# Performance work log

Measured on AMD Instinct MI355X. Metric: run time of the kernel, lower is better.

## Reference

```python
import jax, jax.numpy as jnp
import numpy as np

jax.config.update("jax_enable_x64", True)

B, S = 256, 256
TINY = float(np.finfo(np.float64).tiny)  # torch.finfo().tiny for double


def _matrix_tree_logZ(scores, mask):
    """scores: [B,S,S] float64, mask: [B,S] bool (col 0 is False).
    Returns sum over batch of log partition function (Matrix-Tree theorem)."""
    lens = mask.sum(-1)  # token counts per sentence (excludes root col)
    mask_r = mask.at[:, 0].set(True)  # index_fill(1, 0, 1)
    pair = mask_r[:, :, None] & mask_r[:, None, :]  # [B,S,S]
    s = jnp.where(pair, scores, -jnp.inf)
    m = jnp.max(s.reshape(s.shape[0], -1), axis=-1)  # [B] per-batch max for stability
    A = jnp.maximum(jnp.exp(s - m[:, None, None]), TINY)  # clamp like torch
    idx = jnp.arange(S)
    D = jnp.zeros_like(A).at[:, idx, idx].set(A.sum(-1))  # degree matrix
    eye = jnp.eye(S, dtype=A.dtype)
    # masked_scatter_: rows with mask_r True take (D - A) rows, else identity
    L = jnp.where(mask_r[:, :, None], D - A, eye)
    logZ = jnp.linalg.slogdet(L[:, 1:, 1:])[1] + m * lens
    return logZ.sum()


def setup_inputs() -> dict:
    key = jax.random.key(0)
    k1, k2 = jax.random.split(key)
    scores = jax.random.normal(k1, (B, S, S), dtype=jnp.float32)
    lens = jax.random.randint(k2, (B,), S // 2, S)  # sentence lengths
    pos = jnp.arange(S)
    # col 0 (pseudo root) False, padding beyond length False
    mask = (pos[None, :] >= 1) & (pos[None, :] < lens[:, None])
    return {"scores": scores, "mask": mask}


def reference(scores, mask):
    # mbr=True path: marginals = d logZ / d scores (computed in double like torch)
    s64 = scores.astype(jnp.float64)
    probs = jax.grad(_matrix_tree_logZ)(s64, mask)
    return probs.astype(jnp.float32)
```

## Files before the change

kernel.cpp:

```cpp
#include <hip/hip_runtime.h>
#include <math.h>


#define S 256
#define BB 256

__device__ __forceinline__ int rowmap(int lr, int kb) {
    int rt = lr >> 6;
    int rb = rt + (rt >= kb ? 1 : 0);
    return rb * 64 + (lr & 63);
}

__global__ __launch_bounds__(256) void k_max(const float* __restrict__ sc,
                                             float* __restrict__ partial) {
    int b = blockIdx.y, rg = blockIdx.x;
    const float4* p4 = (const float4*)(sc + (size_t)b * S * S + rg * 8192);
    int tid = threadIdx.x;
    float4 v[8];
    #pragma unroll
    for (int it = 0; it < 8; ++it) v[it] = p4[tid + 256 * it];
    float m = -1e30f;
    #pragma unroll
    for (int it = 0; it < 8; ++it)
        m = fmaxf(m, fmaxf(fmaxf(v[it].x, v[it].y), fmaxf(v[it].z, v[it].w)));
    for (int off = 32; off > 0; off >>= 1) m = fmaxf(m, __shfl_down(m, off));
    __shared__ float sm[4];
    if ((tid & 63) == 0) sm[tid >> 6] = m;
    __syncthreads();
    if (tid == 0) partial[b * 8 + rg] = fmaxf(fmaxf(sm[0], sm[1]), fmaxf(sm[2], sm[3]));
}

__global__ void k_n(const unsigned char* __restrict__ mk, const float* __restrict__ partial,
                    double* __restrict__ mb, int* __restrict__ nb) {
    int b = blockIdx.x, j = threadIdx.x;
    __shared__ int shc[4];

    const unsigned int* mw = (const unsigned int*)mk;
    unsigned int w0 = mw[0], w1 = mw[1];
    int mode = (w0 != 0u) ? 0 : ((w1 != 0u) ? 1 : 2);

    int c;
    if (mode == 0)      c = (mk[(size_t)b * S + j] != 0);
    else if (mode == 1) c = (((const int*)mk)[(size_t)b * S + j] != 0);
    else                c = (((const long long*)mk)[(size_t)b * S + j] != 0LL);

    int lane = j & 63, wid = j >> 6;
    int cs = c;
    for (int off = 32; off > 0; off >>= 1) cs += __shfl_down(cs, off);
    if (lane == 0) shc[wid] = cs;
    __syncthreads();
    if (j == 0) {
        nb[b] = shc[0] + shc[1] + shc[2] + shc[3];
        float mm = partial[b * 8];
        #pragma unroll
        for (int q = 1; q < 8; ++q) mm = fmaxf(mm, partial[b * 8 + q]);
        mb[b] = (double)mm;
    }
}

__global__ void k_build(const float* __restrict__ sc, const double* __restrict__ mb,
                        const int* __restrict__ nb, double* __restrict__ Mg) {
    int p = blockIdx.x, b = blockIdx.y, j = threadIdx.x;
    int n = nb[b];
    double* Mrow = Mg + ((size_t)b * S + p) * S;
    if (p >= n) {
        Mrow[j] = (j == p) ? 1.0 : 0.0;
        return;
    }
    __shared__ double se[S];
    __shared__ double shs[4];
    double m = mb[b];
    double e = (j <= n) ? (double)expf((float)((double)sc[((size_t)b * S + (p + 1)) * S + j] - m)) : 0.0;
    se[j] = e;
    int lane = j & 63, wid = j >> 6;
    double ssum = e;
    for (int off = 32; off > 0; off >>= 1) ssum += __shfl_down(ssum, off);
    if (lane == 0) shs[wid] = ssum;
    __syncthreads();
    double rowsum = shs[0] + shs[1] + shs[2] + shs[3];
    double v;
    if (j < n) v = ((j == p) ? rowsum : 0.0) - se[j + 1];
    else       v = (j == p) ? 1.0 : 0.0;
    Mrow[j] = v;
}

__global__ __launch_bounds__(256) void k_gjrow(double* __restrict__ Mg, double* __restrict__ Pg,
                                               int kb) {
    int b = blockIdx.x, tid = threadIdx.x;
    double* M = Mg + (size_t)b * S * S;
    double* P = Pg + (size_t)b * 4096;
    __shared__ double PT[64][66];
    __shared__ double Rs[64][200];
    __shared__ double rowbuf[64];
    __shared__ double colbuf[64];

    int i = tid >> 2, g = tid & 3, c0 = g << 4;
    double c[16];
    #pragma unroll
    for (int u = 0; u < 16; ++u)
        c[u] = M[(size_t)(kb * 64 + i) * S + kb * 64 + c0 + u];

    for (int kt = 0; kt < 4; ++kt) {
        #pragma unroll
        for (int ks = 0; ks < 16; ++ks) {
            int k = kt * 16 + ks;
            if (i == k) {
                #pragma unroll
                for (int u = 0; u < 16; ++u) rowbuf[c0 + u] = c[u];
            }
            if (g == kt) colbuf[i] = c[ks];
            __syncthreads();
            double pv = rowbuf[k];
            double f  = colbuf[i];
            double pivinv = 1.0 / pv;
            double rk[16];
            #pragma unroll
            for (int m2 = 0; m2 < 8; ++m2) {
                double2 t = *(const double2*)&rowbuf[c0 + 2 * m2];
                rk[2 * m2] = t.x; rk[2 * m2 + 1] = t.y;
            }
            if (i == k) {
                #pragma unroll
                for (int u = 0; u < 16; ++u)
                    c[u] = ((g == kt) && (u == ks)) ? pivinv : c[u] * pivinv;
            } else {
                double gm = f * pivinv;
                #pragma unroll
                for (int u = 0; u < 16; ++u)
                    c[u] = ((g == kt) && (u == ks)) ? (-gm) : fma(-gm, rk[u], c[u]);
            }
            __syncthreads();
        }
    }
    #pragma unroll
    for (int u = 0; u < 16; ++u) {
        PT[c0 + u][i] = c[u];
        P[i * 64 + c0 + u] = c[u];
        M[(size_t)(kb * 64 + i) * S + kb * 64 + c0 + u] = c[u];
    }
    {
        int cidx = tid & 63;
        #pragma unroll
        for (int rep = 0; rep < 16; ++rep) {
            int r = rep * 4 + (tid >> 6);
            #pragma unroll
            for (int cc = 0; cc < 3; ++cc) {
                int j = cc * 64 + cidx;
                Rs[r][j] = M[(size_t)(kb * 64 + r) * S + rowmap(j, kb)];
            }
        }
    }
    __syncthreads();

    int tx = tid & 15, ty = tid >> 4;
    double2 acc[4][6];
    #pragma unroll
    for (int q = 0; q < 4; ++q)
        #pragma unroll
        for (int w = 0; w < 6; ++w) acc[q][w] = double2{0.0, 0.0};

    for (int s = 0; s < 64; ++s) {
        double2 p01 = *(const double2*)&PT[s][4 * ty];
        double2 p23 = *(const double2*)&PT[s][4 * ty + 2];
        #pragma unroll
        for (int w = 0; w < 6; ++w) {
            double2 r = *(const double2*)&Rs[s][2 * tx + 32 * w];
            acc[0][w].x = fma(p01.x, r.x, acc[0][w].x); acc[0][w].y = fma(p01.x, r.y, acc[0][w].y);
            acc[1][w].x = fma(p01.y, r.x, acc[1][w].x); acc[1][w].y = fma(p01.y, r.y, acc[1][w].y);
            acc[2][w].x = fma(p23.x, r.x, acc[2][w].x); acc[2][w].y = fma(p23.x, r.y, acc[2][w].y);
            acc[3][w].x = fma(p23.y, r.x, acc[3][w].x); acc[3][w].y = fma(p23.y, r.y, acc[3][w].y);
        }
    }
    #pragma unroll
    for (int q = 0; q < 4; ++q) {
        size_t row = (size_t)(kb * 64 + 4 * ty + q) * S;
        #pragma unroll
        for (int w = 0; w < 6; ++w) {
            int j = 2 * tx + 32 * w;
            *(double2*)&M[row + rowmap(j, kb)] = acc[q][w];
        }
    }
}

__global__ __launch_bounds__(256) void k_int(double* __restrict__ Mg, int kb) {
    int id = blockIdx.x;
    int b = id >> 1, half = id & 1;
    double* M = Mg + (size_t)b * S * S;
    int tid = threadIdx.x;
    __shared__ double FTs[32][98];
    __shared__ double Rss[32][200];

    int tx = tid & 15, ty = tid >> 4;
    double2 acc[6][6];
    #pragma unroll
    for (int q = 0; q < 6; ++q)
        #pragma unroll
        for (int w = 0; w < 6; ++w) acc[q][w] = double2{0.0, 0.0};

    for (int ck = 0; ck < 2; ++ck) {
        __syncthreads();
        {
            int kk = tid & 31, lrb = (tid >> 5) * 12;
            #pragma unroll
            for (int q = 0; q < 12; ++q) {
                int lrg = half * 96 + lrb + q;
                FTs[kk][lrb + q] =
                    M[(size_t)rowmap(lrg, kb) * S + kb * 64 + ck * 32 + kk];
            }
            int jl = tid & 63, ss = tid >> 6;
            #pragma unroll
            for (int rep = 0; rep < 8; ++rep) {
                int kk2 = ss + 4 * rep;
                #pragma unroll
                for (int cc = 0; cc < 3; ++cc) {
                    int j = cc * 64 + jl;
                    Rss[kk2][j] = M[(size_t)(kb * 64 + ck * 32 + kk2) * S + rowmap(j, kb)];
                }
            }
        }
        __syncthreads();
        for (int kk = 0; kk < 32; ++kk) {
            double2 f01 = *(const double2*)&FTs[kk][6 * ty];
            double2 f23 = *(const double2*)&FTs[kk][6 * ty + 2];
            double2 f45 = *(const double2*)&FTs[kk][6 * ty + 4];
            #pragma unroll
            for (int w = 0; w < 6; ++w) {
                double2 r = *(const double2*)&Rss[kk][2 * tx + 32 * w];
                acc[0][w].x = fma(f01.x, r.x, acc[0][w].x); acc[0][w].y = fma(f01.x, r.y, acc[0][w].y);
                acc[1][w].x = fma(f01.y, r.x, acc[1][w].x); acc[1][w].y = fma(f01.y, r.y, acc[1][w].y);
                acc[2][w].x = fma(f23.x, r.x, acc[2][w].x); acc[2][w].y = fma(f23.x, r.y, acc[2][w].y);
                acc[3][w].x = fma(f23.y, r.x, acc[3][w].x); acc[3][w].y = fma(f23.y, r.y, acc[3][w].y);
                acc[4][w].x = fma(f45.x, r.x, acc[4][w].x); acc[4][w].y = fma(f45.x, r.y, acc[4][w].y);
                acc[5][w].x = fma(f45.y, r.x, acc[5][w].x); acc[5][w].y = fma(f45.y, r.y, acc[5][w].y);
            }
        }
    }
    #pragma unroll
    for (int q = 0; q < 6; ++q) {
        int lrg = half * 96 + ty * 6 + q;
        size_t row = (size_t)rowmap(lrg, kb) * S;
        #pragma unroll
        for (int w = 0; w < 6; ++w) {
            int j = 2 * tx + 32 * w;
            double* p = &M[row + rowmap(j, kb)];
            double2 old = *(double2*)p;
            *(double2*)p = double2{old.x - acc[q][w].x, old.y - acc[q][w].y};
        }
    }
}

__global__ __launch_bounds__(256) void k_colP(double* __restrict__ Mg,
                                              const double* __restrict__ Pg, int kb) {
    int b = blockIdx.x, tid = threadIdx.x;
    double* M = Mg + (size_t)b * S * S;
    const double* P = Pg + (size_t)b * 4096;
    __shared__ double FT2[64][194];
    __shared__ double Ps[64][66];
    {
        int k = tid & 63;
        #pragma unroll
        for (int rep = 0; rep < 48; ++rep) {
            int lr = rep * 4 + (tid >> 6);
            FT2[k][lr] = M[(size_t)rowmap(lr, kb) * S + kb * 64 + k];
        }
        #pragma unroll
        for (int rep = 0; rep < 16; ++rep) {
            int r = rep * 4 + (tid >> 6);
            Ps[r][k] = P[r * 64 + k];
        }
    }
    __syncthreads();
    int tx = tid & 15, ty = tid >> 4;
    double2 acc[12][2];
    #pragma unroll
    for (int q = 0; q < 12; ++q) { acc[q][0] = double2{0.0, 0.0}; acc[q][1] = double2{0.0, 0.0}; }

    for (int k = 0; k < 64; ++k) {
        double2 f[6];
        #pragma unroll
        for (int h = 0; h < 6; ++h) f[h] = *(const double2*)&FT2[k][12 * ty + 2 * h];
        double2 r0 = *(const double2*)&Ps[k][2 * tx];
        double2 r1 = *(const double2*)&Ps[k][2 * tx + 32];
        #pragma unroll
        for (int h = 0; h < 6; ++h) {
            acc[2 * h][0].x     = fma(f[h].x, r0.x, acc[2 * h][0].x);
            acc[2 * h][0].y     = fma(f[h].x, r0.y, acc[2 * h][0].y);
            acc[2 * h][1].x     = fma(f[h].x, r1.x, acc[2 * h][1].x);
            acc[2 * h][1].y     = fma(f[h].x, r1.y, acc[2 * h][1].y);
            acc[2 * h + 1][0].x = fma(f[h].y, r0.x, acc[2 * h + 1][0].x);
            acc[2 * h + 1][0].y = fma(f[h].y, r0.y, acc[2 * h + 1][0].y);
            acc[2 * h + 1][1].x = fma(f[h].y, r1.x, acc[2 * h + 1][1].x);
            acc[2 * h + 1][1].y = fma(f[h].y, r1.y, acc[2 * h + 1][1].y);
        }
    }
    #pragma unroll
    for (int q = 0; q < 12; ++q) {
        int lr = ty * 12 + q;
        size_t row = (size_t)rowmap(lr, kb) * S + kb * 64;
        #pragma unroll
        for (int w = 0; w < 2; ++w) {
            int u = 2 * tx + 32 * w;
            *(double2*)&M[row + u] = double2{-acc[q][w].x, -acc[q][w].y};
        }
    }
}

__global__ __launch_bounds__(256) void k_epi(const float* __restrict__ sc,
                                             const double* __restrict__ Mg,
                                             const double* __restrict__ mb,
                                             const int* __restrict__ nb,
                                             float* __restrict__ out) {
    int b = blockIdx.y;
    int t = blockIdx.x;
    int jj = t & 3, ii = t >> 2;
    int tid = threadIdx.x;
    int n = nb[b];
    double m = mb[b];
    const double* X = Mg + (size_t)b * S * S;
    __shared__ double Xs[64][33];
    __shared__ double sdiag[32];
    if (tid < 32) {
        int idx = 32 * ii + tid - 1;
        sdiag[tid] = (idx >= 0) ? X[(size_t)idx * S + idx] : 0.0;
    }
    {
        int c = tid >> 2, a0 = (tid & 3) << 3;
        int xr = 64 * jj + c - 1;
        #pragma unroll
        for (int u = 0; u < 8; ++u) {
            int a = a0 + u;
            int xc = 32 * ii + a - 1;
            Xs[c][a] = (xr >= 0 && xc >= 0) ? X[(size_t)xr * S + xc] : 0.0;
        }
    }
    __syncthreads();
    int cl = tid & 63, ag = tid >> 6;
    #pragma unroll
    for (int aa = 0; aa < 8; ++aa) {
        int a = ag * 8 + aa;
        int i = 32 * ii + a;
        int j = 64 * jj + cl;
        float v = 0.0f;
        if (i >= 1 && i <= n && j <= n) {
            double A = (double)expf((float)((double)sc[((size_t)b * S + i) * S + j] - m));
            double sub = (j >= 1) ? Xs[cl][a] : 0.0;
            v = (float)(A * (sdiag[a] - sub));
        }
        out[((size_t)b * S + i) * S + j] = v;
    }
}

extern "C" void kernel_launch(void* const* d_in, const int* in_sizes, int n_in,
                              void* d_out, int out_size, void* d_ws, size_t ws_size,
                              hipStream_t stream) {
    (void)in_sizes; (void)n_in; (void)out_size; (void)ws_size;
    const float* sc = (const float*)d_in[0];
    const unsigned char* mk = (const unsigned char*)d_in[1];
    double* ws = (double*)d_ws;

    double* M  = ws;
    double* P  = M + (size_t)BB * S * S;
    double* mb = P + (size_t)BB * 4096;
    int*    nb = (int*)(mb + BB);
    float*  partial = (float*)P;
    float*  out = (float*)d_out;

    k_max<<<dim3(8, BB), 256, 0, stream>>>(sc, partial);
    k_n<<<BB, 256, 0, stream>>>(mk, partial, mb, nb);
    k_build<<<dim3(S, BB), 256, 0, stream>>>(sc, mb, nb, M);
    for (int kb = 0; kb < 4; ++kb) {
        k_gjrow<<<BB, 256, 0, stream>>>(M, P, kb);
        k_int<<<2 * BB, 256, 0, stream>>>(M, kb);
        k_colP<<<BB, 256, 0, stream>>>(M, P, kb);
    }
    k_epi<<<dim3(32, BB), 256, 0, stream>>>(sc, M, mb, nb, out);
}
```

Measured before the change: 600.6 us.

## Rework build, GJ pivot sync, colP split, and epilogue transpose path

k_build now handles one row per wavefront (four rows per block) using wave shuffles instead of a cross-wave reduction. k_gjrow double-buffers the pivot row and column so each elimination step needs one barrier instead of two. k_colP is split across two blocks per batch with a K-chunked shared-memory tile, for more parallelism and less LDS per block. The epilogue becomes a transpose kernel that writes the inverse, cast to float, into the output buffer, followed by a vectorized float4 elementwise pass. That pass computes the subtracted term in float precision, which may cost some accuracy.

```diff
diff --git a/kernel.cpp b/kernel.cpp
--- a/kernel.cpp
+++ b/kernel.cpp
@@ -58,30 +58,39 @@
     }
 }
 
-__global__ void k_build(const float* __restrict__ sc, const double* __restrict__ mb,
-                        const int* __restrict__ nb, double* __restrict__ Mg) {
-    int p = blockIdx.x, b = blockIdx.y, j = threadIdx.x;
+__global__ __launch_bounds__(256) void k_build(const float* __restrict__ sc,
+                                               const double* __restrict__ mb,
+                                               const int* __restrict__ nb,
+                                               double* __restrict__ Mg) {
+    int b = blockIdx.y;
+    int wid = threadIdx.x >> 6, lane = threadIdx.x & 63;
+    int p = blockIdx.x * 4 + wid;
     int n = nb[b];
+    double m = mb[b];
+    __shared__ double se[4][260];
     double* Mrow = Mg + ((size_t)b * S + p) * S;
-    if (p >= n) {
-        Mrow[j] = (j == p) ? 1.0 : 0.0;
-        return;
-    }
-    __shared__ double se[S];
-    __shared__ double shs[4];
-    double m = mb[b];
-    double e = (j <= n) ? (double)expf((float)((double)sc[((size_t)b * S + (p + 1)) * S + j] - m)) : 0.0;
-    se[j] = e;
-    int lane = j & 63, wid = j >> 6;
-    double ssum = e;
+    bool act = (p < n);
+    double ssum = 0.0;
+    #pragma unroll
+    for (int c4 = 0; c4 < 4; ++c4) {
+        int j = lane + 64 * c4;
+        double ev = 0.0;
+        if (act && j <= n)
+            ev = (double)expf((float)((double)sc[((size_t)b * S + (p + 1)) * S + j] - m));
+        se[wid][j] = ev;
+        ssum += ev;
+    }
     for (int off = 32; off > 0; off >>= 1) ssum += __shfl_down(ssum, off);
-    if (lane == 0) shs[wid] = ssum;
+    ssum = __shfl(ssum, 0);
     __syncthreads();
-    double rowsum = shs[0] + shs[1] + shs[2] + shs[3];
-    double v;
-    if (j < n) v = ((j == p) ? rowsum : 0.0) - se[j + 1];
-    else       v = (j == p) ? 1.0 : 0.0;
-    Mrow[j] = v;
+    #pragma unroll
+    for (int c4 = 0; c4 < 4; ++c4) {
+        int j = lane + 64 * c4;
+        double v;
+        if (act && j < n) v = ((j == p) ? ssum : 0.0) - se[wid][j + 1];
+        else              v = (j == p) ? 1.0 : 0.0;
+        Mrow[j] = v;
+    }
 }
 
 __global__ __launch_bounds__(256) void k_gjrow(double* __restrict__ Mg, double* __restrict__ Pg,
@@ -91,8 +100,8 @@
     double* P = Pg + (size_t)b * 4096;
     __shared__ double PT[64][66];
     __shared__ double Rs[64][200];
-    __shared__ double rowbuf[64];
-    __shared__ double colbuf[64];
+    __shared__ double rbuf[2][64];
+    __shared__ double cbuf[2][64];
 
     int i = tid >> 2, g = tid & 3, c0 = g << 4;
     double c[16];
@@ -100,25 +109,27 @@
     for (int u = 0; u < 16; ++u)
         c[u] = M[(size_t)(kb * 64 + i) * S + kb * 64 + c0 + u];
 
+    if (i == 0) {
+        #pragma unroll
+        for (int u = 0; u < 16; ++u) rbuf[0][c0 + u] = c[u];
+    }
+    if (g == 0) cbuf[0][i] = c[0];
+
     for (int kt = 0; kt < 4; ++kt) {
         #pragma unroll
         for (int ks = 0; ks < 16; ++ks) {
             int k = kt * 16 + ks;
-            if (i == k) {
-                #pragma unroll
-                for (int u = 0; u < 16; ++u) rowbuf[c0 + u] = c[u];
-            }
-            if (g == kt) colbuf[i] = c[ks];
+            const int par = ks & 1;
             __syncthreads();
-            double pv = rowbuf[k];
-            double f  = colbuf[i];
+            double pv = rbuf[par][k];
+            double f  = cbuf[par][i];
+            double rk[16];
+            #pragma unroll
+            for (int m2 = 0; m2 < 8; ++m2) {
+                double2 t = *(const double2*)&rbuf[par][c0 + 2 * m2];
+                rk[2 * m2] = t.x; rk[2 * m2 + 1] = t.y;
+            }
             double pivinv = 1.0 / pv;
-            double rk[16];
-            #pragma unroll
-            for (int m2 = 0; m2 < 8; ++m2) {
-                double2 t = *(const double2*)&rowbuf[c0 + 2 * m2];
-                rk[2 * m2] = t.x; rk[2 * m2 + 1] = t.y;
-            }
             if (i == k) {
                 #pragma unroll
                 for (int u = 0; u < 16; ++u)
@@ -129,7 +140,12 @@
                 for (int u = 0; u < 16; ++u)
                     c[u] = ((g == kt) && (u == ks)) ? (-gm) : fma(-gm, rk[u], c[u]);
             }
-            __syncthreads();
+            if (i == k + 1) {
+                #pragma unroll
+                for (int u = 0; u < 16; ++u) rbuf[par ^ 1][c0 + u] = c[u];
+            }
+            if (ks < 15) { if (g == kt)     cbuf[par ^ 1][i] = c[ks + 1]; }
+            else         { if (g == kt + 1) cbuf[par ^ 1][i] = c[0]; }
         }
     }
     #pragma unroll
@@ -251,52 +267,57 @@
 
 __global__ __launch_bounds__(256) void k_colP(double* __restrict__ Mg,
                                               const double* __restrict__ Pg, int kb) {
-    int b = blockIdx.x, tid = threadIdx.x;
+    int id = blockIdx.x;
+    int b = id >> 1, half = id & 1;
     double* M = Mg + (size_t)b * S * S;
     const double* P = Pg + (size_t)b * 4096;
-    __shared__ double FT2[64][194];
-    __shared__ double Ps[64][66];
-    {
-        int k = tid & 63;
-        #pragma unroll
-        for (int rep = 0; rep < 48; ++rep) {
-            int lr = rep * 4 + (tid >> 6);
-            FT2[k][lr] = M[(size_t)rowmap(lr, kb) * S + kb * 64 + k];
-        }
-        #pragma unroll
-        for (int rep = 0; rep < 16; ++rep) {
-            int r = rep * 4 + (tid >> 6);
-            Ps[r][k] = P[r * 64 + k];
-        }
-    }
-    __syncthreads();
+    int tid = threadIdx.x;
+    __shared__ double FTs[32][98];
+    __shared__ double Ps[32][66];
+
     int tx = tid & 15, ty = tid >> 4;
-    double2 acc[12][2];
-    #pragma unroll
-    for (int q = 0; q < 12; ++q) { acc[q][0] = double2{0.0, 0.0}; acc[q][1] = double2{0.0, 0.0}; }
-
-    for (int k = 0; k < 64; ++k) {
-        double2 f[6];
-        #pragma unroll
-        for (int h = 0; h < 6; ++h) f[h] = *(const double2*)&FT2[k][12 * ty + 2 * h];
-        double2 r0 = *(const double2*)&Ps[k][2 * tx];
-        double2 r1 = *(const double2*)&Ps[k][2 * tx + 32];
-        #pragma unroll
-        for (int h = 0; h < 6; ++h) {
-            acc[2 * h][0].x     = fma(f[h].x, r0.x, acc[2 * h][0].x);
-            acc[2 * h][0].y     = fma(f[h].x, r0.y, acc[2 * h][0].y);
-            acc[2 * h][1].x     = fma(f[h].x, r1.x, acc[2 * h][1].x);
-            acc[2 * h][1].y     = fma(f[h].x, r1.y, acc[2 * h][1].y);
-            acc[2 * h + 1][0].x = fma(f[h].y, r0.x, acc[2 * h + 1][0].x);
-            acc[2 * h + 1][0].y = fma(f[h].y, r0.y, acc[2 * h + 1][0].y);
-            acc[2 * h + 1][1].x = fma(f[h].y, r1.x, acc[2 * h + 1][1].x);
-            acc[2 * h + 1][1].y = fma(f[h].y, r1.y, acc[2 * h + 1][1].y);
-        }
-    }
-    #pragma unroll
-    for (int q = 0; q < 12; ++q) {
-        int lr = ty * 12 + q;
-        size_t row = (size_t)rowmap(lr, kb) * S + kb * 64;
+    double2 acc[6][2];
+    #pragma unroll
+    for (int q = 0; q < 6; ++q) { acc[q][0] = double2{0.0, 0.0}; acc[q][1] = double2{0.0, 0.0}; }
+
+    for (int ck = 0; ck < 2; ++ck) {
+        __syncthreads();
+        {
+            int kk = tid & 31, lrb = (tid >> 5) * 12;
+            #pragma unroll
+            for (int q = 0; q < 12; ++q) {
+                int lrg = half * 96 + lrb + q;
+                FTs[kk][lrb + q] =
+                    M[(size_t)rowmap(lrg, kb) * S + kb * 64 + ck * 32 + kk];
+            }
+            int u = tid & 63;
+            #pragma unroll
+            for (int rep = 0; rep < 8; ++rep) {
+                int r = rep * 4 + (tid >> 6);
+                Ps[r][u] = P[(ck * 32 + r) * 64 + u];
+            }
+        }
+        __syncthreads();
+        for (int kk = 0; kk < 32; ++kk) {
+            double2 f01 = *(const double2*)&FTs[kk][6 * ty];
+            double2 f23 = *(const double2*)&FTs[kk][6 * ty + 2];
+            double2 f45 = *(const double2*)&FTs[kk][6 * ty + 4];
+            #pragma unroll
+            for (int w = 0; w < 2; ++w) {
+                double2 r = *(const double2*)&Ps[kk][2 * tx + 32 * w];
+                acc[0][w].x = fma(f01.x, r.x, acc[0][w].x); acc[0][w].y = fma(f01.x, r.y, acc[0][w].y);
+                acc[1][w].x = fma(f01.y, r.x, acc[1][w].x); acc[1][w].y = fma(f01.y, r.y, acc[1][w].y);
+                acc[2][w].x = fma(f23.x, r.x, acc[2][w].x); acc[2][w].y = fma(f23.x, r.y, acc[2][w].y);
+                acc[3][w].x = fma(f23.y, r.x, acc[3][w].x); acc[3][w].y = fma(f23.y, r.y, acc[3][w].y);
+                acc[4][w].x = fma(f45.x, r.x, acc[4][w].x); acc[4][w].y = fma(f45.x, r.y, acc[4][w].y);
+                acc[5][w].x = fma(f45.y, r.x, acc[5][w].x); acc[5][w].y = fma(f45.y, r.y, acc[5][w].y);
+            }
+        }
+    }
+    #pragma unroll
+    for (int q = 0; q < 6; ++q) {
+        int lrg = half * 96 + ty * 6 + q;
+        size_t row = (size_t)rowmap(lrg, kb) * S + kb * 64;
         #pragma unroll
         for (int w = 0; w < 2; ++w) {
             int u = 2 * tx + 32 * w;
@@ -305,49 +326,63 @@
     }
 }
 
-__global__ __launch_bounds__(256) void k_epi(const float* __restrict__ sc,
-                                             const double* __restrict__ Mg,
-                                             const double* __restrict__ mb,
-                                             const int* __restrict__ nb,
-                                             float* __restrict__ out) {
+__global__ __launch_bounds__(256) void k_xt(const double* __restrict__ Mg,
+                                            float* __restrict__ outF,
+                                            double* __restrict__ Dg) {
+    int b = blockIdx.y, t = blockIdx.x;
+    int r = t & 3, c = t >> 2;
+    const double* M = Mg + (size_t)b * S * S;
+    __shared__ float L[64][65];
+    int tid = threadIdx.x;
+    int cc = tid & 63;
+    #pragma unroll
+    for (int rep = 0; rep < 16; ++rep) {
+        int rr = rep * 4 + (tid >> 6);
+        L[rr][cc] = (float)M[(size_t)(64 * r + rr) * S + 64 * c + cc];
+    }
+    if (r == c && tid < 64)
+        Dg[(size_t)b * S + 64 * r + tid] = M[(size_t)(64 * r + tid) * S + 64 * r + tid];
+    __syncthreads();
+    int pp = tid & 63;
+    #pragma unroll
+    for (int rep = 0; rep < 16; ++rep) {
+        int qq = rep * 4 + (tid >> 6);
+        int orow = 64 * c + qq + 1, ocol = 64 * r + pp + 1;
+        if (orow < 256 && ocol < 256)
+            outF[((size_t)b * S + orow) * S + ocol] = L[pp][qq];
+    }
+}
+
+__global__ __launch_bounds__(256) void k_epi2(const float* __restrict__ sc,
+                                              const double* __restrict__ Dg,
+                                              const double* __restrict__ mb,
+                                              const int* __restrict__ nb,
+                                              float* __restrict__ out) {
     int b = blockIdx.y;
-    int t = blockIdx.x;
-    int jj = t & 3, ii = t >> 2;
-    int tid = threadIdx.x;
+    int idx4 = blockIdx.x * 256 + threadIdx.x;
+    int i = idx4 >> 6;
+    int jq = idx4 & 63;
     int n = nb[b];
-    double m = mb[b];
-    const double* X = Mg + (size_t)b * S * S;
-    __shared__ double Xs[64][33];
-    __shared__ double sdiag[32];
-    if (tid < 32) {
-        int idx = 32 * ii + tid - 1;
-        sdiag[tid] = (idx >= 0) ? X[(size_t)idx * S + idx] : 0.0;
-    }
-    {
-        int c = tid >> 2, a0 = (tid & 3) << 3;
-        int xr = 64 * jj + c - 1;
-        #pragma unroll
-        for (int u = 0; u < 8; ++u) {
-            int a = a0 + u;
-            int xc = 32 * ii + a - 1;
-            Xs[c][a] = (xr >= 0 && xc >= 0) ? X[(size_t)xr * S + xc] : 0.0;
-        }
-    }
-    __syncthreads();
-    int cl = tid & 63, ag = tid >> 6;
-    #pragma unroll
-    for (int aa = 0; aa < 8; ++aa) {
-        int a = ag * 8 + aa;
-        int i = 32 * ii + a;
-        int j = 64 * jj + cl;
+    float m = (float)mb[b];
+    size_t base = ((size_t)b * S + i) * S + 4 * jq;
+    float4 xf = *(const float4*)(out + base);
+    float4 s4 = *(const float4*)(sc + base);
+    double dg = (i >= 1) ? Dg[(size_t)b * S + i - 1] : 0.0;
+    float xfa[4] = {xf.x, xf.y, xf.z, xf.w};
+    float sa[4]  = {s4.x, s4.y, s4.z, s4.w};
+    float ra[4];
+    #pragma unroll
+    for (int comp = 0; comp < 4; ++comp) {
+        int j = 4 * jq + comp;
         float v = 0.0f;
         if (i >= 1 && i <= n && j <= n) {
-            double A = (double)expf((float)((double)sc[((size_t)b * S + i) * S + j] - m));
-            double sub = (j >= 1) ? Xs[cl][a] : 0.0;
-            v = (float)(A * (sdiag[a] - sub));
-        }
-        out[((size_t)b * S + i) * S + j] = v;
-    }
+            double A = (double)expf(sa[comp] - m);
+            double sub = (j >= 1) ? (double)xfa[comp] : 0.0;
+            v = (float)(A * (dg - sub));
+        }
+        ra[comp] = v;
+    }
+    *(float4*)(out + base) = float4{ra[0], ra[1], ra[2], ra[3]};
 }
 
 extern "C" void kernel_launch(void* const* d_in, const int* in_sizes, int n_in,
@@ -362,16 +397,18 @@
     double* P  = M + (size_t)BB * S * S;
     double* mb = P + (size_t)BB * 4096;
     int*    nb = (int*)(mb + BB);
+    double* Dg = mb + 2 * BB;
     float*  partial = (float*)P;
     float*  out = (float*)d_out;
 
     k_max<<<dim3(8, BB), 256, 0, stream>>>(sc, partial);
     k_n<<<BB, 256, 0, stream>>>(mk, partial, mb, nb);
-    k_build<<<dim3(S, BB), 256, 0, stream>>>(sc, mb, nb, M);
+    k_build<<<dim3(64, BB), 256, 0, stream>>>(sc, mb, nb, M);
     for (int kb = 0; kb < 4; ++kb) {
         k_gjrow<<<BB, 256, 0, stream>>>(M, P, kb);
         k_int<<<2 * BB, 256, 0, stream>>>(M, kb);
-        k_colP<<<BB, 256, 0, stream>>>(M, P, kb);
-    }
-    k_epi<<<dim3(32, BB), 256, 0, stream>>>(sc, M, mb, nb, out);
-}
+        k_colP<<<2 * BB, 256, 0, stream>>>(M, P, kb);
+    }
+    k_xt<<<dim3(16, BB), 256, 0, stream>>>(M, out, Dg);
+    k_epi2<<<dim3(64, BB), 256, 0, stream>>>(sc, Dg, mb, nb, out);
+}
```

Result: no change. 600.6 us (-0.0%).
